# Kernel optimization log

Measured on AMD Instinct MI355X. Metric: run time of the kernel, lower is better.

The kernel has to match this reference:

```python
import jax, jax.numpy as jnp
import numpy as np

N, FP, H, E, B = 60000, 120, 512, 3, 600
NNZ = 5_000_000
NFORCE = 3 * N
ELEMENTS = jnp.array([1, 8, 29], dtype=jnp.int32)  # unique_atoms (H, O, Cu)


def setup_inputs():
    key = jax.random.key(0)
    ks = jax.random.split(key, 10)
    fingerprints = jax.random.normal(ks[0], (N, FP), jnp.float32)
    atomic_numbers = ELEMENTS[jax.random.randint(ks[1], (N,), 0, E)]
    image_idx = jnp.sort(jax.random.randint(ks[2], (N,), 0, B)).astype(jnp.int32)
    W1 = jax.random.normal(ks[3], (E, FP, H), jnp.float32) / np.float32(np.sqrt(FP))
    b1 = jnp.zeros((E, H), jnp.float32)
    W2 = jax.random.normal(ks[4], (E, H, H), jnp.float32) / np.float32(np.sqrt(H))
    b2 = jnp.zeros((E, H), jnp.float32)
    W3 = jax.random.normal(ks[5], (E, H, 1), jnp.float32) / np.float32(np.sqrt(H))
    b3 = jnp.zeros((E, 1), jnp.float32)
    # sparse fprimes [N*FP, 3*N] in COO form
    fprime_rows = jax.random.randint(ks[6], (NNZ,), 0, N * FP).astype(jnp.int32)
    fprime_cols = jax.random.randint(ks[7], (NNZ,), 0, NFORCE).astype(jnp.int32)
    fprime_vals = jax.random.normal(ks[8], (NNZ,), jnp.float32) * 0.01
    return {"fingerprints": fingerprints, "atomic_numbers": atomic_numbers,
            "image_idx": image_idx, "W1": W1, "b1": b1, "W2": W2, "b2": b2,
            "W3": W3, "b3": b3, "fprime_rows": fprime_rows,
            "fprime_cols": fprime_cols, "fprime_vals": fprime_vals}


def _energy(fingerprints, W1, b1, W2, b2, W3, b3, mask, image_idx):
    # stacked per-element 3-layer tanh MLPs, evaluated densely over all atoms
    h = jnp.tanh(jnp.einsum('nf,efh->enh', fingerprints, W1) + b1[:, None, :])
    h = jnp.tanh(jnp.einsum('enh,ehk->enk', h, W2) + b2[:, None, :])
    out = jnp.einsum('enh,eho->eno', h, W3) + b3[:, None, :]  # [E, N, 1]
    o = jnp.sum(mask.T * out[..., 0], axis=0)  # mask-select per-atom energy [N]
    return jax.ops.segment_sum(o, image_idx, num_segments=B)  # per-image energy [B]


def reference(fingerprints, atomic_numbers, image_idx, W1, b1, W2, b2, W3, b3,
              fprime_rows, fprime_cols, fprime_vals):
    # ElementMask: one-hot over unique atomic numbers
    mask = (atomic_numbers[:, None] == ELEMENTS[None, :]).astype(fingerprints.dtype)  # [N, E]
    efn = lambda fp: _energy(fp, W1, b1, W2, b2, W3, b3, mask, image_idx)
    energy, vjp_fn = jax.vjp(efn, fingerprints)
    # grad of energy wrt fingerprints with grad_outputs = ones
    g = vjp_fn(jnp.ones_like(energy))[0].reshape(-1)  # [N*FP]
    # forces = -fprimes^T @ g  via sparse scatter
    forces = -jax.ops.segment_sum(fprime_vals * g[fprime_rows], fprime_cols,
                                  num_segments=NFORCE).reshape(-1, 3)  # [N, 3]
    return (energy, forces)
```

## Files before the change

### kernel.cpp

```cpp
#include <hip/hip_runtime.h>

#define N_ATOMS 60000
#define FPD 120
#define HD 512
#define EE 3
#define BB 600
#define NNZ_C 5000000
#define NFORCE (3 * N_ATOMS)
#define TB 32
#define CBITS 12
#define NBUCK ((NFORCE + 4095) / 4096)
#define NSLOT 16

typedef unsigned short ushort_t;
typedef unsigned int uint_t;
typedef unsigned long long u64_t;
typedef __attribute__((ext_vector_type(8))) __bf16 bf16x8;
typedef __attribute__((ext_vector_type(4))) float f32x4;
typedef __attribute__((ext_vector_type(4))) int i32x4;

union BF8 { f32x4 f; bf16x8 h; };

__device__ __forceinline__ ushort_t f2bf(float x) {
    uint_t u = __builtin_bit_cast(uint_t, x);
    u = (u + 0x7FFFu + ((u >> 16) & 1u)) >> 16;
    return (ushort_t)u;
}
__device__ __forceinline__ float bf2f(ushort_t s) {
    uint_t u = ((uint_t)s) << 16;
    return __builtin_bit_cast(float, u);
}
__device__ __forceinline__ float fast_tanh(float x) {
    float e2 = __expf(2.f * x);
    return fmaf(-2.f, __frcp_rn(e2 + 1.f), 1.f);
}

__global__ __launch_bounds__(256) void build_lists(const int* __restrict__ z,
                                                   int* __restrict__ counts,
                                                   int* __restrict__ lists) {
    __shared__ int lc[3];
    __shared__ int lbase[3];
    const int t = threadIdx.x;
    if (t < 3) lc[t] = 0;
    __syncthreads();
    const int i = blockIdx.x * 256 + t;
    int e = 0, pos = 0;
    if (i < N_ATOMS) {
        int zi = z[i];
        e = (zi == 1) ? 0 : ((zi == 8) ? 1 : 2);
        pos = atomicAdd(&lc[e], 1);
    }
    __syncthreads();
    if (t < 3) lbase[t] = atomicAdd(&counts[t], lc[t]);
    __syncthreads();
    if (i < N_ATOMS) lists[e * N_ATOMS + lbase[e] + pos] = i;
}

#define R_W2 (EE * 16 * 32 * 512)
#define R_W1 (EE * 4 * 32 * 512)
#define R_W1T (EE * 16 * 8 * 512)
__global__ __launch_bounds__(256) void pack_all(
    const float* __restrict__ W1, const float* __restrict__ W2,
    ushort_t* __restrict__ W1p, ushort_t* __restrict__ W2p,
    ushort_t* __restrict__ W2Tp, ushort_t* __restrict__ W1Tp) {
    int idx = blockIdx.x * 256 + threadIdx.x;
    if (idx < R_W2) {
        int p = idx;
        int j = p & 7, L = (p >> 3) & 63, ct = (p >> 9) & 31, ks = (p >> 14) & 15, e = p >> 18;
        int k = ks * 32 + ((L >> 4) << 3) + j;
        int n = (ct << 4) + (L & 15);
        W2p[p]  = f2bf(W2[((e << 9) + k) * 512 + n]);
        W2Tp[p] = f2bf(W2[((e << 9) + n) * 512 + k]);
    } else if (idx < R_W2 + R_W1) {
        int p = idx - R_W2;
        int j = p & 7, L = (p >> 3) & 63, ct = (p >> 9) & 31, ks = (p >> 14) & 3, e = p >> 16;
        int k = ks * 32 + ((L >> 4) << 3) + j;
        int n = (ct << 4) + (L & 15);
        W1p[p] = (k < FPD) ? f2bf(W1[(e * FPD + k) * 512 + n]) : (ushort_t)0;
    } else if (idx < R_W2 + R_W1 + R_W1T) {
        int p = idx - R_W2 - R_W1;
        int j = p & 7, L = (p >> 3) & 63, ct = (p >> 9) & 7, ks = (p >> 12) & 15, e = p >> 16;
        int k = ks * 32 + ((L >> 4) << 3) + j;
        int n = (ct << 4) + (L & 15);
        W1Tp[p] = (n < FPD) ? f2bf(W1[(e * FPD + n) * 512 + k]) : (ushort_t)0;
    }
}

#define STR 520
#define FSTR 136

__global__ __launch_bounds__(512, 4) void mlp_mfma(
    const float* __restrict__ fps, const int* __restrict__ image_idx,
    const float* __restrict__ b1, const float* __restrict__ b2,
    const float* __restrict__ W3, const float* __restrict__ b3,
    const ushort_t* __restrict__ W1p, const ushort_t* __restrict__ W2p,
    const ushort_t* __restrict__ W2Tp, const ushort_t* __restrict__ W1Tp,
    const int* __restrict__ counts, const int* __restrict__ lists,
    float* __restrict__ energy, ushort_t* __restrict__ g) {
    __shared__ ushort_t sH1[TB * STR];
    __shared__ ushort_t sD[TB * STR];
    __shared__ float sW3[512];
    __shared__ float eAcc[TB];
    __shared__ int sAtom[TB];
    __shared__ int sImg[TB];

    const int e = blockIdx.x % EE;
    const int tile = blockIdx.x / EE;
    const int cnt = counts[e];
    const int base = tile * TB;
    if (base >= cnt) return;
    const int nA = min(TB, cnt - base);
    const int* lst = lists + e * N_ATOMS + base;

    const int t = threadIdx.x;
    const int w = t >> 6, lane = t & 63, quad = lane >> 4, lc = lane & 15;

    if (t < TB) {
        int a = (t < nA) ? lst[t] : -1;
        sAtom[t] = a;
        sImg[t] = (a >= 0) ? image_idx[a] : 0;
        eAcc[t] = 0.f;
    }
    if (t < 512) sW3[t] = W3[e * 512 + t];
    for (int i = t; i < TB * 128; i += 512) {
        int a = i >> 7, f = i & 127;
        float v = 0.f;
        if (f < FPD && a < nA) v = __builtin_nontemporal_load(&fps[(long long)lst[a] * FPD + f]);
        sD[a * FSTR + f] = f2bf(v);
    }
    __syncthreads();

    float b1c[4], b2c[4];
#pragma unroll
    for (int c = 0; c < 4; c++) {
        int col = w * 64 + c * 16 + lc;
        b1c[c] = b1[e * 512 + col];
        b2c[c] = b2[e * 512 + col];
    }

    f32x4 acc[2][4];

#pragma unroll
    for (int rt = 0; rt < 2; rt++)
#pragma unroll
        for (int c = 0; c < 4; c++) acc[rt][c] = (f32x4)0.f;
    {
        const ushort_t* wbase = W1p + ((size_t)(e * 4) * 32 + w * 4) * 512 + lane * 8;
        BF8 bb[4][4];
#pragma unroll
        for (int ks = 0; ks < 4; ks++)
#pragma unroll
            for (int c = 0; c < 4; c++)
                bb[ks][c].f = *(const f32x4*)(wbase + ((size_t)ks * 32 + c) * 512);
#pragma unroll
        for (int ks = 0; ks < 4; ks++) {
            bf16x8 a0 = *(const bf16x8*)((const char*)sD + lc * (FSTR * 2) + ks * 64 + quad * 16);
            bf16x8 a1 = *(const bf16x8*)((const char*)sD + (16 + lc) * (FSTR * 2) + ks * 64 + quad * 16);
#pragma unroll
            for (int c = 0; c < 4; c++) {
                acc[0][c] = __builtin_amdgcn_mfma_f32_16x16x32_bf16(a0, bb[ks][c].h, acc[0][c], 0, 0, 0);
                acc[1][c] = __builtin_amdgcn_mfma_f32_16x16x32_bf16(a1, bb[ks][c].h, acc[1][c], 0, 0, 0);
            }
        }
    }
#pragma unroll
    for (int c = 0; c < 4; c++) {
        int col = w * 64 + c * 16 + lc;
#pragma unroll
        for (int rt = 0; rt < 2; rt++)
#pragma unroll
            for (int r = 0; r < 4; r++) {
                int row = rt * 16 + quad * 4 + r;
                sH1[row * STR + col] = f2bf(fast_tanh(acc[rt][c][r] + b1c[c]));
            }
    }
    __syncthreads();

#pragma unroll
    for (int rt = 0; rt < 2; rt++)
#pragma unroll
        for (int c = 0; c < 4; c++) acc[rt][c] = (f32x4)0.f;
    {
        const ushort_t* wbase = W2p + ((size_t)(e * 16) * 32 + w * 4) * 512 + lane * 8;
#pragma unroll
        for (int ksc = 0; ksc < 4; ksc++) {
            BF8 bb[4][4];
#pragma unroll
            for (int kk = 0; kk < 4; kk++)
#pragma unroll
                for (int c = 0; c < 4; c++)
                    bb[kk][c].f = *(const f32x4*)(wbase + (size_t)(ksc * 4 + kk) * 32 * 512 + (size_t)c * 512);
#pragma unroll
            for (int kk = 0; kk < 4; kk++) {
                int ks = ksc * 4 + kk;
                bf16x8 a0 = *(const bf16x8*)((const char*)sH1 + lc * (STR * 2) + ks * 64 + quad * 16);
                bf16x8 a1 = *(const bf16x8*)((const char*)sH1 + (16 + lc) * (STR * 2) + ks * 64 + quad * 16);
#pragma unroll
                for (int c = 0; c < 4; c++) {
                    acc[0][c] = __builtin_amdgcn_mfma_f32_16x16x32_bf16(a0, bb[kk][c].h, acc[0][c], 0, 0, 0);
                    acc[1][c] = __builtin_amdgcn_mfma_f32_16x16x32_bf16(a1, bb[kk][c].h, acc[1][c], 0, 0, 0);
                }
            }
        }
    }
    {
        float ep[2][4];
#pragma unroll
        for (int rt = 0; rt < 2; rt++)
#pragma unroll
            for (int r = 0; r < 4; r++) ep[rt][r] = 0.f;
#pragma unroll
        for (int c = 0; c < 4; c++) {
            int col = w * 64 + c * 16 + lc;
            float w3c = sW3[col];
#pragma unroll
            for (int rt = 0; rt < 2; rt++)
#pragma unroll
                for (int r = 0; r < 4; r++) {
                    int row = rt * 16 + quad * 4 + r;
                    float h2 = fast_tanh(acc[rt][c][r] + b2c[c]);
                    ep[rt][r] += h2 * w3c;
                    sD[row * STR + col] = f2bf(w3c * (1.f - h2 * h2));
                }
        }
#pragma unroll
        for (int rt = 0; rt < 2; rt++)
#pragma unroll
            for (int r = 0; r < 4; r++) {
                float p = ep[rt][r];
                p += __shfl_xor(p, 1);
                p += __shfl_xor(p, 2);
                p += __shfl_xor(p, 4);
                p += __shfl_xor(p, 8);
                if (lc == 0) atomicAdd(&eAcc[rt * 16 + quad * 4 + r], p);
            }
    }
    __syncthreads();

    if (t < nA) atomicAdd(&energy[sImg[t]], eAcc[t] + b3[e]);

#pragma unroll
    for (int rt = 0; rt < 2; rt++)
#pragma unroll
        for (int c = 0; c < 4; c++) acc[rt][c] = (f32x4)0.f;
    {
        const ushort_t* wbase = W2Tp + ((size_t)(e * 16) * 32 + w * 4) * 512 + lane * 8;
#pragma unroll
        for (int ksc = 0; ksc < 4; ksc++) {
            BF8 bb[4][4];
#pragma unroll
            for (int kk = 0; kk < 4; kk++)
#pragma unroll
                for (int c = 0; c < 4; c++)
                    bb[kk][c].f = *(const f32x4*)(wbase + (size_t)(ksc * 4 + kk) * 32 * 512 + (size_t)c * 512);
#pragma unroll
            for (int kk = 0; kk < 4; kk++) {
                int ks = ksc * 4 + kk;
                bf16x8 a0 = *(const bf16x8*)((const char*)sD + lc * (STR * 2) + ks * 64 + quad * 16);
                bf16x8 a1 = *(const bf16x8*)((const char*)sD + (16 + lc) * (STR * 2) + ks * 64 + quad * 16);
#pragma unroll
                for (int c = 0; c < 4; c++) {
                    acc[0][c] = __builtin_amdgcn_mfma_f32_16x16x32_bf16(a0, bb[kk][c].h, acc[0][c], 0, 0, 0);
                    acc[1][c] = __builtin_amdgcn_mfma_f32_16x16x32_bf16(a1, bb[kk][c].h, acc[1][c], 0, 0, 0);
                }
            }
        }
    }
#pragma unroll
    for (int c = 0; c < 4; c++) {
        int col = w * 64 + c * 16 + lc;
#pragma unroll
        for (int rt = 0; rt < 2; rt++)
#pragma unroll
            for (int r = 0; r < 4; r++) {
                int row = rt * 16 + quad * 4 + r;
                float h1v = bf2f(sH1[row * STR + col]);
                acc[rt][c][r] *= (1.f - h1v * h1v);
            }
    }
    __syncthreads();
#pragma unroll
    for (int c = 0; c < 4; c++) {
        int col = w * 64 + c * 16 + lc;
#pragma unroll
        for (int rt = 0; rt < 2; rt++)
#pragma unroll
            for (int r = 0; r < 4; r++) {
                int row = rt * 16 + quad * 4 + r;
                sH1[row * STR + col] = f2bf(acc[rt][c][r]);
            }
    }
    __syncthreads();

    f32x4 acc7[2];
#pragma unroll
    for (int rt = 0; rt < 2; rt++) acc7[rt] = (f32x4)0.f;
    {
        const ushort_t* wbase = W1Tp + ((size_t)(e * 16) * 8 + w) * 512 + lane * 8;
#pragma unroll
        for (int ksc = 0; ksc < 2; ksc++) {
            BF8 bb[8];
#pragma unroll
            for (int kk = 0; kk < 8; kk++)
                bb[kk].f = *(const f32x4*)(wbase + (size_t)(ksc * 8 + kk) * 8 * 512);
#pragma unroll
            for (int kk = 0; kk < 8; kk++) {
                int ks = ksc * 8 + kk;
                bf16x8 a0 = *(const bf16x8*)((const char*)sH1 + lc * (STR * 2) + ks * 64 + quad * 16);
                bf16x8 a1 = *(const bf16x8*)((const char*)sH1 + (16 + lc) * (STR * 2) + ks * 64 + quad * 16);
                acc7[0] = __builtin_amdgcn_mfma_f32_16x16x32_bf16(a0, bb[kk].h, acc7[0], 0, 0, 0);
                acc7[1] = __builtin_amdgcn_mfma_f32_16x16x32_bf16(a1, bb[kk].h, acc7[1], 0, 0, 0);
            }
        }
    }
    {
        int col = w * 16 + lc;
#pragma unroll
        for (int rt = 0; rt < 2; rt++)
#pragma unroll
            for (int r = 0; r < 4; r++) {
                int row = rt * 16 + quad * 4 + r;
                if (col < FPD && row < nA)
                    g[(long long)sAtom[row] * FPD + col] = f2bf(acc7[rt][r]);
            }
    }
}

__global__ __launch_bounds__(256) void bucket_hist(const int* __restrict__ cols,
                                                   int* __restrict__ bcnt) {
    __shared__ int h[NBUCK];
    const int t = threadIdx.x;
    if (t < NBUCK) h[t] = 0;
    __syncthreads();
    const int nv = NNZ_C / 4;
    for (int vk = blockIdx.x * 256 + t; vk < nv; vk += gridDim.x * 256) {
        i32x4 c = __builtin_nontemporal_load((const i32x4*)cols + vk);
        atomicAdd(&h[c.x >> CBITS], 1);
        atomicAdd(&h[c.y >> CBITS], 1);
        atomicAdd(&h[c.z >> CBITS], 1);
        atomicAdd(&h[c.w >> CBITS], 1);
    }
    __syncthreads();
    if (t < NBUCK) atomicAdd(&bcnt[t], h[t]);
}

__global__ void bucket_scan(const int* __restrict__ bcnt, int* __restrict__ bbase,
                            int* __restrict__ bcur) {
    if (threadIdx.x == 0 && blockIdx.x == 0) {
        int s = 0;
        for (int i = 0; i < NBUCK; i++) { bbase[i] = s; bcur[i] = s; s += bcnt[i]; }
    }
}

__global__ __launch_bounds__(256) void bucket_scatter(
    const int* __restrict__ rows, const int* __restrict__ cols,
    const float* __restrict__ vals, int* __restrict__ bcur,
    u64_t* __restrict__ bpack) {
    __shared__ int lcnt[NBUCK];
    __shared__ int lcur[NBUCK];
    const int t = threadIdx.x;
    if (t < NBUCK) lcnt[t] = 0;
    __syncthreads();
    const int vk0 = blockIdx.x * 2048;
    i32x4 ccache[8];
    int nb[8][4];
#pragma unroll
    for (int i = 0; i < 8; i++) {
        int vk = vk0 + i * 256 + t;
        if (vk * 4 < NNZ_C) {
            i32x4 c = __builtin_nontemporal_load((const i32x4*)cols + vk);
            ccache[i] = c;
            nb[i][0] = c.x >> CBITS; nb[i][1] = c.y >> CBITS;
            nb[i][2] = c.z >> CBITS; nb[i][3] = c.w >> CBITS;
            atomicAdd(&lcnt[nb[i][0]], 1);
            atomicAdd(&lcnt[nb[i][1]], 1);
            atomicAdd(&lcnt[nb[i][2]], 1);
            atomicAdd(&lcnt[nb[i][3]], 1);
        } else {
            nb[i][0] = -1;
        }
    }
    __syncthreads();
    if (t < NBUCK) lcur[t] = atomicAdd(&bcur[t], lcnt[t]);
    __syncthreads();
#pragma unroll
    for (int i = 0; i < 8; i++) {
        int vk = vk0 + i * 256 + t;
        if (vk * 4 < NNZ_C) {
            i32x4 r = __builtin_nontemporal_load((const i32x4*)rows + vk);
            f32x4 v = __builtin_nontemporal_load((const f32x4*)vals + vk);
            int rr[4] = {r.x, r.y, r.z, r.w};
            int cc[4] = {ccache[i].x, ccache[i].y, ccache[i].z, ccache[i].w};
            float vv[4] = {v.x, v.y, v.z, v.w};
#pragma unroll
            for (int u = 0; u < 4; u++) {
                int pos = atomicAdd(&lcur[nb[i][u]], 1);
                u64_t pk = (u64_t)(uint_t)rr[u] |
                           ((u64_t)(uint_t)(cc[u] & ((1 << CBITS) - 1)) << 23) |
                           ((u64_t)f2bf(vv[u]) << 35);
                bpack[pos] = pk;
            }
        }
    }
}

__global__ __launch_bounds__(256) void scatter_lds(
    const u64_t* __restrict__ bpack, const int* __restrict__ bbase,
    const int* __restrict__ bcnt, const ushort_t* __restrict__ g,
    float* __restrict__ forcesP) {
    __shared__ float facc[1 << CBITS];
    const int b = blockIdx.x >> 4;
    const int s = blockIdx.x & (NSLOT - 1);
    const int t = threadIdx.x;
    for (int i = t; i < (1 << CBITS); i += 256) facc[i] = 0.f;
    __syncthreads();
    const int base = bbase[b];
    const int end = base + bcnt[b];
    for (int i = base + s * 256 + t; i < end; i += NSLOT * 256) {
        u64_t pk = bpack[i];
        int r = (int)(pk & 0x7FFFFFu);
        int cin = (int)((pk >> 23) & 0xFFFu);
        float v = bf2f((ushort_t)(pk >> 35));
        atomicAdd(&facc[cin], -v * bf2f(g[r]));
    }
    __syncthreads();
    const int colbase = b << CBITS;
    float* fp = forcesP + (size_t)s * NFORCE;
    for (int i = t; i < (1 << CBITS); i += 256) {
        int col = colbase + i;
        if (col < NFORCE) __builtin_nontemporal_store(facc[i], &fp[col]);
    }
}

__global__ void reduce_forces(const float* __restrict__ forcesP, float* __restrict__ forces) {
    int i = blockIdx.x * blockDim.x + threadIdx.x;
    if (i >= NFORCE) return;
    float s = 0.f;
#pragma unroll
    for (int x = 0; x < NSLOT; x++) s += forcesP[(size_t)x * NFORCE + i];
    forces[i] = s;
}

__global__ __launch_bounds__(256) void scatter_forces(
    const int* __restrict__ rows, const int* __restrict__ cols,
    const float* __restrict__ vals, const ushort_t* __restrict__ g,
    float* __restrict__ forcesP) {
    int k = blockIdx.x * 256 + threadIdx.x;
    if (k >= NNZ_C / 4) return;
    int slot = blockIdx.x & (NSLOT - 1);
    i32x4 r = __builtin_nontemporal_load((const i32x4*)rows + k);
    i32x4 c = __builtin_nontemporal_load((const i32x4*)cols + k);
    f32x4 v = __builtin_nontemporal_load((const f32x4*)vals + k);
    float* fp = forcesP + (size_t)slot * NFORCE;
    atomicAdd(&fp[c.x], -v.x * bf2f(g[r.x]));
    atomicAdd(&fp[c.y], -v.y * bf2f(g[r.y]));
    atomicAdd(&fp[c.z], -v.z * bf2f(g[r.z]));
    atomicAdd(&fp[c.w], -v.w * bf2f(g[r.w]));
}

extern "C" void kernel_launch(void* const* d_in, const int* in_sizes, int n_in,
                              void* d_out, int out_size, void* d_ws, size_t ws_size,
                              hipStream_t stream) {
    const float* fps = (const float*)d_in[0];
    const int* z = (const int*)d_in[1];
    const int* img = (const int*)d_in[2];
    const float* W1 = (const float*)d_in[3];
    const float* b1 = (const float*)d_in[4];
    const float* W2 = (const float*)d_in[5];
    const float* b2 = (const float*)d_in[6];
    const float* W3 = (const float*)d_in[7];
    const float* b3 = (const float*)d_in[8];
    const int* rows = (const int*)d_in[9];
    const int* cols = (const int*)d_in[10];
    const float* vals = (const float*)d_in[11];

    float* out = (float*)d_out;
    float* energy = out;
    float* forces = out + BB;

    char* ws = (char*)d_ws;
    int* counts = (int*)ws;
    int* lists = (int*)(ws + 256);
    ushort_t* W1p = (ushort_t*)(ws + 720384);
    ushort_t* W2p = (ushort_t*)(ws + 1113600);
    ushort_t* W2Tp = (ushort_t*)(ws + 2686464);
    ushort_t* W1Tp = (ushort_t*)(ws + 4259328);
    ushort_t* g = (ushort_t*)(ws + 4652544);
    float* forcesP = (float*)(ws + 19052544);
    int* bmeta = (int*)(ws + 30572544);
    int* bcnt = bmeta, *bbase = bmeta + 64, *bcur = bmeta + 128;
    u64_t* bpack = (u64_t*)(ws + 30573568);
    const size_t WS_NEED = 70573568;
    (void)in_sizes; (void)n_in; (void)out_size;

    (void)hipMemsetAsync(energy, 0, BB * sizeof(float), stream);
    (void)hipMemsetAsync(counts, 0, 256, stream);

    build_lists<<<(N_ATOMS + 255) / 256, 256, 0, stream>>>(z, counts, lists);
    pack_all<<<(R_W2 + R_W1 + R_W1T + 255) / 256, 256, 0, stream>>>(
        W1, W2, W1p, W2p, W2Tp, W1Tp);

    int tiles = (N_ATOMS + TB - 1) / TB;
    mlp_mfma<<<EE * tiles, 512, 0, stream>>>(fps, img, b1, b2, W3, b3,
                                             W1p, W2p, W2Tp, W1Tp,
                                             counts, lists, energy, g);

    if (ws_size >= WS_NEED) {
        (void)hipMemsetAsync(bmeta, 0, 768, stream);
        bucket_hist<<<256, 256, 0, stream>>>(cols, bcnt);
        bucket_scan<<<1, 64, 0, stream>>>(bcnt, bbase, bcur);
        bucket_scatter<<<(NNZ_C + 8191) / 8192, 256, 0, stream>>>(
            rows, cols, vals, bcur, bpack);
        scatter_lds<<<NBUCK * NSLOT, 256, 0, stream>>>(bpack, bbase, bcnt, g, forcesP);
        reduce_forces<<<(NFORCE + 255) / 256, 256, 0, stream>>>(forcesP, forces);
    } else {
        (void)hipMemsetAsync(forcesP, 0, (size_t)NSLOT * NFORCE * sizeof(float), stream);
        scatter_forces<<<(NNZ_C / 4 + 255) / 256, 256, 0, stream>>>(rows, cols, vals, g, forcesP);
        reduce_forces<<<(NFORCE + 255) / 256, 256, 0, stream>>>(forcesP, forces);
    }
}
```

Baseline: 455.7 us.

## Double atoms per MLP tile and software-pipeline weight loads across layers

Raises the per-block atom tile from 32 to 64 rows so each weight fragment loaded from global memory feeds twice as many MFMAs. Weight fragments for W2, W2T and W1T are now double-buffered in registers and prefetched one chunk ahead, including across layer boundaries and before the first barrier, so global load latency overlaps compute. The cost is higher register and LDS use per block; the launch bound drops to 2 blocks per CU and there are half as many blocks, which reduces occupancy and the ability to hide latency.

Result: slower. 484.3 us (+6.3%).

```diff
diff --git a/kernel.cpp b/kernel.cpp
--- a/kernel.cpp
+++ b/kernel.cpp
@@ -7,7 +7,7 @@
 #define BB 600
 #define NNZ_C 5000000
 #define NFORCE (3 * N_ATOMS)
-#define TB 32
+#define TB 64
 #define CBITS 12
 #define NBUCK ((NFORCE + 4095) / 4096)
 #define NSLOT 16
@@ -89,7 +89,54 @@
 #define STR 520
 #define FSTR 136
 
-__global__ __launch_bounds__(512, 4) void mlp_mfma(
+__device__ __forceinline__ void ld_chunk16(BF8 (&bb)[4][4], const ushort_t* wbase, int ksc) {
+#pragma unroll
+    for (int kk = 0; kk < 4; kk++)
+#pragma unroll
+        for (int c = 0; c < 4; c++)
+            bb[kk][c].f = *(const f32x4*)(wbase + ((size_t)(ksc * 4 + kk) * 32 + c) * 512);
+}
+
+__device__ __forceinline__ void mm_chunk16(f32x4 (&acc)[4][4], const BF8 (&bb)[4][4],
+                                           const ushort_t* sA, int ksc,
+                                           int lc, int quad, int rowbytes) {
+#pragma unroll
+    for (int kk = 0; kk < 4; kk++) {
+        int ks = ksc * 4 + kk;
+        bf16x8 a[4];
+#pragma unroll
+        for (int rt = 0; rt < 4; rt++)
+            a[rt] = *(const bf16x8*)((const char*)sA + (rt * 16 + lc) * rowbytes + ks * 64 + quad * 16);
+#pragma unroll
+        for (int c = 0; c < 4; c++)
+#pragma unroll
+            for (int rt = 0; rt < 4; rt++)
+                acc[rt][c] = __builtin_amdgcn_mfma_f32_16x16x32_bf16(a[rt], bb[kk][c].h, acc[rt][c], 0, 0, 0);
+    }
+}
+
+__device__ __forceinline__ void ld_chunk8(BF8 (&bb)[8], const ushort_t* wbase, int ksc) {
+#pragma unroll
+    for (int kk = 0; kk < 8; kk++)
+        bb[kk].f = *(const f32x4*)(wbase + (size_t)(ksc * 8 + kk) * 8 * 512);
+}
+
+__device__ __forceinline__ void mm_chunk8(f32x4 (&acc7)[4], const BF8 (&bb)[8],
+                                          const ushort_t* sA, int ksc, int lc, int quad) {
+#pragma unroll
+    for (int kk = 0; kk < 8; kk++) {
+        int ks = ksc * 8 + kk;
+        bf16x8 a[4];
+#pragma unroll
+        for (int rt = 0; rt < 4; rt++)
+            a[rt] = *(const bf16x8*)((const char*)sA + (rt * 16 + lc) * (STR * 2) + ks * 64 + quad * 16);
+#pragma unroll
+        for (int rt = 0; rt < 4; rt++)
+            acc7[rt] = __builtin_amdgcn_mfma_f32_16x16x32_bf16(a[rt], bb[kk].h, acc7[rt], 0, 0, 0);
+    }
+}
+
+__global__ __launch_bounds__(512, 2) void mlp_mfma(
     const float* __restrict__ fps, const int* __restrict__ image_idx,
     const float* __restrict__ b1, const float* __restrict__ b2,
     const float* __restrict__ W3, const float* __restrict__ b3,
@@ -115,6 +162,18 @@
     const int t = threadIdx.x;
     const int w = t >> 6, lane = t & 63, quad = lane >> 4, lc = lane & 15;
 
+    const ushort_t* w1base = W1p + ((size_t)(e * 4) * 32 + w * 4) * 512 + lane * 8;
+    BF8 bb1[4][4];
+    ld_chunk16(bb1, w1base, 0);
+
+    float b1c[4], b2c[4];
+#pragma unroll
+    for (int c = 0; c < 4; c++) {
+        int col = w * 64 + c * 16 + lc;
+        b1c[c] = b1[e * 512 + col];
+        b2c[c] = b2[e * 512 + col];
+    }
+
     if (t < TB) {
         int a = (t < nA) ? lst[t] : -1;
         sAtom[t] = a;
@@ -130,44 +189,24 @@
     }
     __syncthreads();
 
-    float b1c[4], b2c[4];
+    f32x4 acc[4][4];
+
+#pragma unroll
+    for (int rt = 0; rt < 4; rt++)
+#pragma unroll
+        for (int c = 0; c < 4; c++) acc[rt][c] = (f32x4)0.f;
+    mm_chunk16(acc, bb1, sD, 0, lc, quad, FSTR * 2);
+
+    const ushort_t* w2base = W2p + ((size_t)(e * 16) * 32 + w * 4) * 512 + lane * 8;
+    BF8 bbA[4][4], bbB[4][4];
+    ld_chunk16(bbA, w2base, 0);
+    ld_chunk16(bbB, w2base, 1);
+
 #pragma unroll
     for (int c = 0; c < 4; c++) {
         int col = w * 64 + c * 16 + lc;
-        b1c[c] = b1[e * 512 + col];
-        b2c[c] = b2[e * 512 + col];
-    }
-
-    f32x4 acc[2][4];
-
-#pragma unroll
-    for (int rt = 0; rt < 2; rt++)
-#pragma unroll
-        for (int c = 0; c < 4; c++) acc[rt][c] = (f32x4)0.f;
-    {
-        const ushort_t* wbase = W1p + ((size_t)(e * 4) * 32 + w * 4) * 512 + lane * 8;
-        BF8 bb[4][4];
-#pragma unroll
-        for (int ks = 0; ks < 4; ks++)
-#pragma unroll
-            for (int c = 0; c < 4; c++)
-                bb[ks][c].f = *(const f32x4*)(wbase + ((size_t)ks * 32 + c) * 512);
-#pragma unroll
-        for (int ks = 0; ks < 4; ks++) {
-            bf16x8 a0 = *(const bf16x8*)((const char*)sD + lc * (FSTR * 2) + ks * 64 + quad * 16);
-            bf16x8 a1 = *(const bf16x8*)((const char*)sD + (16 + lc) * (FSTR * 2) + ks * 64 + quad * 16);
-#pragma unroll
-            for (int c = 0; c < 4; c++) {
-                acc[0][c] = __builtin_amdgcn_mfma_f32_16x16x32_bf16(a0, bb[ks][c].h, acc[0][c], 0, 0, 0);
-                acc[1][c] = __builtin_amdgcn_mfma_f32_16x16x32_bf16(a1, bb[ks][c].h, acc[1][c], 0, 0, 0);
-            }
-        }
-    }
-#pragma unroll
-    for (int c = 0; c < 4; c++) {
-        int col = w * 64 + c * 16 + lc;
-#pragma unroll
-        for (int rt = 0; rt < 2; rt++)
+#pragma unroll
+        for (int rt = 0; rt < 4; rt++)
 #pragma unroll
             for (int r = 0; r < 4; r++) {
                 int row = rt * 16 + quad * 4 + r;
@@ -177,36 +216,24 @@
     __syncthreads();
 
 #pragma unroll
-    for (int rt = 0; rt < 2; rt++)
+    for (int rt = 0; rt < 4; rt++)
 #pragma unroll
         for (int c = 0; c < 4; c++) acc[rt][c] = (f32x4)0.f;
+    mm_chunk16(acc, bbA, sH1, 0, lc, quad, STR * 2);
+    ld_chunk16(bbA, w2base, 2);
+    mm_chunk16(acc, bbB, sH1, 1, lc, quad, STR * 2);
+    ld_chunk16(bbB, w2base, 3);
+    mm_chunk16(acc, bbA, sH1, 2, lc, quad, STR * 2);
+    mm_chunk16(acc, bbB, sH1, 3, lc, quad, STR * 2);
+
+    const ushort_t* w2tbase = W2Tp + ((size_t)(e * 16) * 32 + w * 4) * 512 + lane * 8;
+    ld_chunk16(bbA, w2tbase, 0);
+    ld_chunk16(bbB, w2tbase, 1);
+
     {
-        const ushort_t* wbase = W2p + ((size_t)(e * 16) * 32 + w * 4) * 512 + lane * 8;
-#pragma unroll
-        for (int ksc = 0; ksc < 4; ksc++) {
-            BF8 bb[4][4];
-#pragma unroll
-            for (int kk = 0; kk < 4; kk++)
-#pragma unroll
-                for (int c = 0; c < 4; c++)
-                    bb[kk][c].f = *(const f32x4*)(wbase + (size_t)(ksc * 4 + kk) * 32 * 512 + (size_t)c * 512);
-#pragma unroll
-            for (int kk = 0; kk < 4; kk++) {
-                int ks = ksc * 4 + kk;
-                bf16x8 a0 = *(const bf16x8*)((const char*)sH1 + lc * (STR * 2) + ks * 64 + quad * 16);
-                bf16x8 a1 = *(const bf16x8*)((const char*)sH1 + (16 + lc) * (STR * 2) + ks * 64 + quad * 16);
-#pragma unroll
-                for (int c = 0; c < 4; c++) {
-                    acc[0][c] = __builtin_amdgcn_mfma_f32_16x16x32_bf16(a0, bb[kk][c].h, acc[0][c], 0, 0, 0);
-                    acc[1][c] = __builtin_amdgcn_mfma_f32_16x16x32_bf16(a1, bb[kk][c].h, acc[1][c], 0, 0, 0);
-                }
-            }
-        }
-    }
-    {
-        float ep[2][4];
-#pragma unroll
-        for (int rt = 0; rt < 2; rt++)
+        float ep[4][4];
+#pragma unroll
+        for (int rt = 0; rt < 4; rt++)
 #pragma unroll
             for (int r = 0; r < 4; r++) ep[rt][r] = 0.f;
 #pragma unroll
@@ -214,7 +241,7 @@
             int col = w * 64 + c * 16 + lc;
             float w3c = sW3[col];
 #pragma unroll
-            for (int rt = 0; rt < 2; rt++)
+            for (int rt = 0; rt < 4; rt++)
 #pragma unroll
                 for (int r = 0; r < 4; r++) {
                     int row = rt * 16 + quad * 4 + r;
@@ -224,7 +251,7 @@
                 }
         }
 #pragma unroll
-        for (int rt = 0; rt < 2; rt++)
+        for (int rt = 0; rt < 4; rt++)
 #pragma unroll
             for (int r = 0; r < 4; r++) {
                 float p = ep[rt][r];
@@ -240,37 +267,26 @@
     if (t < nA) atomicAdd(&energy[sImg[t]], eAcc[t] + b3[e]);
 
 #pragma unroll
-    for (int rt = 0; rt < 2; rt++)
+    for (int rt = 0; rt < 4; rt++)
 #pragma unroll
         for (int c = 0; c < 4; c++) acc[rt][c] = (f32x4)0.f;
-    {
-        const ushort_t* wbase = W2Tp + ((size_t)(e * 16) * 32 + w * 4) * 512 + lane * 8;
-#pragma unroll
-        for (int ksc = 0; ksc < 4; ksc++) {
-            BF8 bb[4][4];
-#pragma unroll
-            for (int kk = 0; kk < 4; kk++)
-#pragma unroll
-                for (int c = 0; c < 4; c++)
-                    bb[kk][c].f = *(const f32x4*)(wbase + (size_t)(ksc * 4 + kk) * 32 * 512 + (size_t)c * 512);
-#pragma unroll
-            for (int kk = 0; kk < 4; kk++) {
-                int ks = ksc * 4 + kk;
-                bf16x8 a0 = *(const bf16x8*)((const char*)sD + lc * (STR * 2) + ks * 64 + quad * 16);
-                bf16x8 a1 = *(const bf16x8*)((const char*)sD + (16 + lc) * (STR * 2) + ks * 64 + quad * 16);
-#pragma unroll
-                for (int c = 0; c < 4; c++) {
-                    acc[0][c] = __builtin_amdgcn_mfma_f32_16x16x32_bf16(a0, bb[kk][c].h, acc[0][c], 0, 0, 0);
-                    acc[1][c] = __builtin_amdgcn_mfma_f32_16x16x32_bf16(a1, bb[kk][c].h, acc[1][c], 0, 0, 0);
-                }
-            }
-        }
-    }
+    mm_chunk16(acc, bbA, sD, 0, lc, quad, STR * 2);
+    ld_chunk16(bbA, w2tbase, 2);
+    mm_chunk16(acc, bbB, sD, 1, lc, quad, STR * 2);
+    ld_chunk16(bbB, w2tbase, 3);
+    mm_chunk16(acc, bbA, sD, 2, lc, quad, STR * 2);
+    mm_chunk16(acc, bbB, sD, 3, lc, quad, STR * 2);
+
+    const ushort_t* w1tbase = W1Tp + ((size_t)(e * 16) * 8 + w) * 512 + lane * 8;
+    BF8 bb7A[8], bb7B[8];
+    ld_chunk8(bb7A, w1tbase, 0);
+    ld_chunk8(bb7B, w1tbase, 1);
+
 #pragma unroll
     for (int c = 0; c < 4; c++) {
         int col = w * 64 + c * 16 + lc;
 #pragma unroll
-        for (int rt = 0; rt < 2; rt++)
+        for (int rt = 0; rt < 4; rt++)
 #pragma unroll
             for (int r = 0; r < 4; r++) {
                 int row = rt * 16 + quad * 4 + r;
@@ -283,7 +299,7 @@
     for (int c = 0; c < 4; c++) {
         int col = w * 64 + c * 16 + lc;
 #pragma unroll
-        for (int rt = 0; rt < 2; rt++)
+        for (int rt = 0; rt < 4; rt++)
 #pragma unroll
             for (int r = 0; r < 4; r++) {
                 int row = rt * 16 + quad * 4 + r;
@@ -292,31 +308,15 @@
     }
     __syncthreads();
 
-    f32x4 acc7[2];
-#pragma unroll
-    for (int rt = 0; rt < 2; rt++) acc7[rt] = (f32x4)0.f;
-    {
-        const ushort_t* wbase = W1Tp + ((size_t)(e * 16) * 8 + w) * 512 + lane * 8;
-#pragma unroll
-        for (int ksc = 0; ksc < 2; ksc++) {
-            BF8 bb[8];
-#pragma unroll
-            for (int kk = 0; kk < 8; kk++)
-                bb[kk].f = *(const f32x4*)(wbase + (size_t)(ksc * 8 + kk) * 8 * 512);
-#pragma unroll
-            for (int kk = 0; kk < 8; kk++) {
-                int ks = ksc * 8 + kk;
-                bf16x8 a0 = *(const bf16x8*)((const char*)sH1 + lc * (STR * 2) + ks * 64 + quad * 16);
-                bf16x8 a1 = *(const bf16x8*)((const char*)sH1 + (16 + lc) * (STR * 2) + ks * 64 + quad * 16);
-                acc7[0] = __builtin_amdgcn_mfma_f32_16x16x32_bf16(a0, bb[kk].h, acc7[0], 0, 0, 0);
-                acc7[1] = __builtin_amdgcn_mfma_f32_16x16x32_bf16(a1, bb[kk].h, acc7[1], 0, 0, 0);
-            }
-        }
-    }
+    f32x4 acc7[4];
+#pragma unroll
+    for (int rt = 0; rt < 4; rt++) acc7[rt] = (f32x4)0.f;
+    mm_chunk8(acc7, bb7A, sH1, 0, lc, quad);
+    mm_chunk8(acc7, bb7B, sH1, 1, lc, quad);
     {
         int col = w * 16 + lc;
 #pragma unroll
-        for (int rt = 0; rt < 2; rt++)
+        for (int rt = 0; rt < 4; rt++)
 #pragma unroll
             for (int r = 0; r < 4; r++) {
                 int row = rt * 16 + quad * 4 + r;
```

## Fuse sparse bucketing into MLP launch and use fixed-capacity buckets

Applied to the files above, without the earlier changes.

Adds extra blocks to the MLP kernel launch that bin the COO entries by force-column bucket, with one global atomic per bucket per block. The entries go into fixed-capacity bucket regions (BCAP) instead of a histogram/scan/scatter chain, so the bucketing overlaps the MLP compute and two launches disappear. The tanh layer-1 activations are also kept in fp32 registers for the derivative, which drops an LDS reload and the bf16 rounding. Risks are bucket overflow if any bucket exceeds BCAP, more register pressure, and a larger workspace requirement.

Measured after the change: 393.9 us. 1.16x faster.

```diff
diff --git a/kernel.cpp b/kernel.cpp
--- a/kernel.cpp
+++ b/kernel.cpp
@@ -11,6 +11,8 @@
 #define CBITS 12
 #define NBUCK ((NFORCE + 4095) / 4096)
 #define NSLOT 16
+#define BCAP 118000
+#define SCAT_BLOCKS ((NNZ_C / 4 + 4095) / 4096)
 
 typedef unsigned short ushort_t;
 typedef unsigned int uint_t;
@@ -96,23 +98,75 @@
     const ushort_t* __restrict__ W1p, const ushort_t* __restrict__ W2p,
     const ushort_t* __restrict__ W2Tp, const ushort_t* __restrict__ W1Tp,
     const int* __restrict__ counts, const int* __restrict__ lists,
-    float* __restrict__ energy, ushort_t* __restrict__ g) {
+    float* __restrict__ energy, ushort_t* __restrict__ g,
+    const int* __restrict__ rows, const int* __restrict__ cols,
+    const float* __restrict__ vals, int* __restrict__ bcnt,
+    u64_t* __restrict__ bpack, int scatBlocks) {
     __shared__ ushort_t sH1[TB * STR];
     __shared__ ushort_t sD[TB * STR];
     __shared__ float sW3[512];
     __shared__ float eAcc[TB];
     __shared__ int sAtom[TB];
     __shared__ int sImg[TB];
-
-    const int e = blockIdx.x % EE;
-    const int tile = blockIdx.x / EE;
+    __shared__ int sLcnt[NBUCK];
+    __shared__ int sLcur[NBUCK];
+
+    const int t = threadIdx.x;
+
+    if (blockIdx.x < (uint_t)scatBlocks) {
+        const int vk0 = blockIdx.x * 4096;
+        if (t < NBUCK) sLcnt[t] = 0;
+        __syncthreads();
+        i32x4 cc[8];
+#pragma unroll
+        for (int i = 0; i < 8; i++) {
+            int vk = vk0 + i * 512 + t;
+            if (vk < NNZ_C / 4) {
+                i32x4 c = __builtin_nontemporal_load((const i32x4*)cols + vk);
+                cc[i] = c;
+                atomicAdd(&sLcnt[c.x >> CBITS], 1);
+                atomicAdd(&sLcnt[c.y >> CBITS], 1);
+                atomicAdd(&sLcnt[c.z >> CBITS], 1);
+                atomicAdd(&sLcnt[c.w >> CBITS], 1);
+            } else {
+                cc[i].x = -1;
+            }
+        }
+        __syncthreads();
+        if (t < NBUCK) sLcur[t] = t * BCAP + atomicAdd(&bcnt[t], sLcnt[t]);
+        __syncthreads();
+#pragma unroll
+        for (int i = 0; i < 8; i++) {
+            int vk = vk0 + i * 512 + t;
+            if (cc[i].x != -1) {
+                i32x4 r = __builtin_nontemporal_load((const i32x4*)rows + vk);
+                f32x4 v = __builtin_nontemporal_load((const f32x4*)vals + vk);
+                int rr[4] = {r.x, r.y, r.z, r.w};
+                int ccv[4] = {cc[i].x, cc[i].y, cc[i].z, cc[i].w};
+                float vv[4] = {v.x, v.y, v.z, v.w};
+#pragma unroll
+                for (int u = 0; u < 4; u++) {
+                    int b = ccv[u] >> CBITS;
+                    int pos = atomicAdd(&sLcur[b], 1);
+                    u64_t pk = (u64_t)(uint_t)rr[u] |
+                               ((u64_t)(uint_t)(ccv[u] & ((1 << CBITS) - 1)) << 23) |
+                               ((u64_t)f2bf(vv[u]) << 35);
+                    bpack[pos] = pk;
+                }
+            }
+        }
+        return;
+    }
+
+    const int mb = blockIdx.x - scatBlocks;
+    const int e = mb % EE;
+    const int tile = mb / EE;
     const int cnt = counts[e];
     const int base = tile * TB;
     if (base >= cnt) return;
     const int nA = min(TB, cnt - base);
     const int* lst = lists + e * N_ATOMS + base;
 
-    const int t = threadIdx.x;
     const int w = t >> 6, lane = t & 63, quad = lane >> 4, lc = lane & 15;
 
     if (t < TB) {
@@ -139,6 +193,7 @@
     }
 
     f32x4 acc[2][4];
+    float h1f[2][4][4];
 
 #pragma unroll
     for (int rt = 0; rt < 2; rt++)
@@ -171,7 +226,9 @@
 #pragma unroll
             for (int r = 0; r < 4; r++) {
                 int row = rt * 16 + quad * 4 + r;
-                sH1[row * STR + col] = f2bf(fast_tanh(acc[rt][c][r] + b1c[c]));
+                float hv = fast_tanh(acc[rt][c][r] + b1c[c]);
+                h1f[rt][c][r] = hv;
+                sH1[row * STR + col] = f2bf(hv);
             }
     }
     __syncthreads();
@@ -267,17 +324,14 @@
         }
     }
 #pragma unroll
-    for (int c = 0; c < 4; c++) {
-        int col = w * 64 + c * 16 + lc;
+    for (int c = 0; c < 4; c++)
 #pragma unroll
         for (int rt = 0; rt < 2; rt++)
 #pragma unroll
             for (int r = 0; r < 4; r++) {
-                int row = rt * 16 + quad * 4 + r;
-                float h1v = bf2f(sH1[row * STR + col]);
-                acc[rt][c][r] *= (1.f - h1v * h1v);
-            }
-    }
+                float hv = h1f[rt][c][r];
+                acc[rt][c][r] *= (1.f - hv * hv);
+            }
     __syncthreads();
 #pragma unroll
     for (int c = 0; c < 4; c++) {
@@ -323,6 +377,33 @@
                 if (col < FPD && row < nA)
                     g[(long long)sAtom[row] * FPD + col] = f2bf(acc7[rt][r]);
             }
+    }
+}
+
+__global__ __launch_bounds__(256) void scatter_lds_cap(
+    const u64_t* __restrict__ bpack, const int* __restrict__ bcnt,
+    const ushort_t* __restrict__ g, float* __restrict__ forcesP) {
+    __shared__ float facc[1 << CBITS];
+    const int b = blockIdx.x >> 4;
+    const int s = blockIdx.x & (NSLOT - 1);
+    const int t = threadIdx.x;
+    for (int i = t; i < (1 << CBITS); i += 256) facc[i] = 0.f;
+    __syncthreads();
+    const int base = b * BCAP;
+    const int end = base + bcnt[b];
+    for (int i = base + s * 256 + t; i < end; i += NSLOT * 256) {
+        u64_t pk = bpack[i];
+        int r = (int)(pk & 0x7FFFFFu);
+        int cin = (int)((pk >> 23) & 0xFFFu);
+        float v = bf2f((ushort_t)(pk >> 35));
+        atomicAdd(&facc[cin], -v * bf2f(g[r]));
+    }
+    __syncthreads();
+    const int colbase = b << CBITS;
+    float* fp = forcesP + (size_t)s * NFORCE;
+    for (int i = t; i < (1 << CBITS); i += 256) {
+        int col = colbase + i;
+        if (col < NFORCE) __builtin_nontemporal_store(facc[i], &fp[col]);
     }
 }
 
@@ -490,6 +571,7 @@
     int* bmeta = (int*)(ws + 30572544);
     int* bcnt = bmeta, *bbase = bmeta + 64, *bcur = bmeta + 128;
     u64_t* bpack = (u64_t*)(ws + 30573568);
+    const size_t WS_FAST = 30573568ull + (size_t)NBUCK * BCAP * 8;
     const size_t WS_NEED = 70573568;
     (void)in_sizes; (void)n_in; (void)out_size;
 
@@ -501,12 +583,21 @@
         W1, W2, W1p, W2p, W2Tp, W1Tp);
 
     int tiles = (N_ATOMS + TB - 1) / TB;
-    mlp_mfma<<<EE * tiles, 512, 0, stream>>>(fps, img, b1, b2, W3, b3,
-                                             W1p, W2p, W2Tp, W1Tp,
-                                             counts, lists, energy, g);
-
-    if (ws_size >= WS_NEED) {
+
+    if (ws_size >= WS_FAST) {
         (void)hipMemsetAsync(bmeta, 0, 768, stream);
+        mlp_mfma<<<SCAT_BLOCKS + EE * tiles, 512, 0, stream>>>(
+            fps, img, b1, b2, W3, b3, W1p, W2p, W2Tp, W1Tp,
+            counts, lists, energy, g,
+            rows, cols, vals, bcnt, bpack, SCAT_BLOCKS);
+        scatter_lds_cap<<<NBUCK * NSLOT, 256, 0, stream>>>(bpack, bcnt, g, forcesP);
+        reduce_forces<<<(NFORCE + 255) / 256, 256, 0, stream>>>(forcesP, forces);
+    } else if (ws_size >= WS_NEED) {
+        (void)hipMemsetAsync(bmeta, 0, 768, stream);
+        mlp_mfma<<<EE * tiles, 512, 0, stream>>>(
+            fps, img, b1, b2, W3, b3, W1p, W2p, W2Tp, W1Tp,
+            counts, lists, energy, g,
+            rows, cols, vals, bcnt, bpack, 0);
         bucket_hist<<<256, 256, 0, stream>>>(cols, bcnt);
         bucket_scan<<<1, 64, 0, stream>>>(bcnt, bbase, bcur);
         bucket_scatter<<<(NNZ_C + 8191) / 8192, 256, 0, stream>>>(
@@ -515,6 +606,10 @@
         reduce_forces<<<(NFORCE + 255) / 256, 256, 0, stream>>>(forcesP, forces);
     } else {
         (void)hipMemsetAsync(forcesP, 0, (size_t)NSLOT * NFORCE * sizeof(float), stream);
+        mlp_mfma<<<EE * tiles, 512, 0, stream>>>(
+            fps, img, b1, b2, W3, b3, W1p, W2p, W2Tp, W1Tp,
+            counts, lists, energy, g,
+            rows, cols, vals, bcnt, (u64_t*)forcesP , 0);
         scatter_forces<<<(NNZ_C / 4 + 255) / 256, 256, 0, stream>>>(rows, cols, vals, g, forcesP);
         reduce_forces<<<(NFORCE + 255) / 256, 256, 0, stream>>>(forcesP, forces);
     }
```
